# Optimization experiments

Measured on AMD Instinct MI355X. Metric: run time of the kernel, lower is better.

Reference implementation:

```python
import jax, jax.numpy as jnp
import numpy as np
from jax import lax


def conv2d(x, w, b, pad):
    # x: NCHW, w: OIHW
    out = lax.conv_general_dilated(x, w, (1, 1), [(pad, pad), (pad, pad)],
                                   dimension_numbers=('NCHW', 'OIHW', 'NCHW'))
    return out + b[None, :, None, None]


def traj_grid_sample(ps, gx, gy):
    """Faithful F.grid_sample (5D, trilinear, zeros padding, align_corners=False)
    applied to ps expanded along a depth axis of size L. Since every depth slice
    of the expanded input equals ps, we gather 2D from ps and fold the z-axis
    interpolation weights / bounds mask in analytically (no (B,C,L,H,W) expand).
    ps: (B,C,H,W); gx, gy: (B,L,H,W) pixel-coordinate flow fields."""
    B, C, H, W = ps.shape
    L = gx.shape[1]
    dt = ps.dtype
    # the original normalizes to [-1,1] assuming align_corners-style ranges
    gxn = gx / (W - 1) * 2 - 1
    gyn = gy / (H - 1) * 2 - 1
    gzn = jnp.arange(1, L + 1, dtype=dt) / (L - 1) * 2 - 1  # (L,)
    # torch grid_sample default align_corners=False unnormalization
    ix = ((gxn + 1) * W - 1) / 2
    iy = ((gyn + 1) * H - 1) / 2
    iz = jnp.broadcast_to((((gzn + 1) * L - 1) / 2)[None, :, None, None], ix.shape)
    x0 = jnp.floor(ix)
    y0 = jnp.floor(iy)
    z0 = jnp.floor(iz)
    bidx = jnp.arange(B)[:, None, None, None]
    out = jnp.zeros((B, L, H, W, C), dtype=dt)
    for dz in (0.0, 1.0):
        zc = z0 + dz
        wz = 1.0 - jnp.abs(iz - zc)
        mz = (zc >= 0) & (zc <= L - 1)
        for dy in (0.0, 1.0):
            yc = y0 + dy
            wy = 1.0 - jnp.abs(iy - yc)
            my = (yc >= 0) & (yc <= H - 1)
            yci = jnp.clip(yc, 0, H - 1).astype(jnp.int32)
            for dx in (0.0, 1.0):
                xc = x0 + dx
                wx = 1.0 - jnp.abs(ix - xc)
                mx = (xc >= 0) & (xc <= W - 1)
                xci = jnp.clip(xc, 0, W - 1).astype(jnp.int32)
                w = wz * wy * wx * (mz & my & mx).astype(dt)  # (B,L,H,W)
                val = ps[bidx, :, yci, xci]  # (B,L,H,W,C)
                out = out + val * w[..., None]
    return jnp.transpose(out, (0, 4, 1, 2, 3))  # (B,C,L,H,W)


def reference(x, prev_state, sub_w1, sub_b1, sub_w2, sub_b2,
              reset_w, reset_b, update_w, update_b, out_w, out_b,
              reset_ww, reset_wb, update_ww, update_wb, out_ww, out_wb):
    B, Ch, H, W = prev_state.shape
    L = sub_w2.shape[0] // 2
    # subCNN: flow generation
    s = jnp.concatenate([x, prev_state], axis=1)
    o = jax.nn.relu(conv2d(s, sub_w1, sub_b1, 2))
    o = jax.nn.relu(conv2d(o, sub_w2, sub_b2, 2))
    M = traj_grid_sample(prev_state, o[:, :L], o[:, L:])  # (B,Ch,L,H,W)
    Mf = M.reshape(B, Ch * L, H, W)  # view(B, C*L, H, W)
    update = jax.nn.sigmoid(conv2d(x, update_w, update_b, 1) + conv2d(Mf, update_ww, update_wb, 0))
    reset = jax.nn.sigmoid(conv2d(x, reset_w, reset_b, 1) + conv2d(Mf, reset_ww, reset_wb, 0))
    v = conv2d(x, out_w, out_b, 1) + reset * conv2d(Mf, out_ww, out_wb, 0)
    out_inputs = jnp.where(v >= 0, v, 0.2 * v)  # leaky_relu(0.2)
    return prev_state * update + out_inputs * (1.0 - update)


def setup_inputs() -> dict:
    key = jax.random.key(0)
    ks = jax.random.split(key, 12)
    B, Cin, Ch, L, H, W = 4, 8, 96, 13, 96, 96
    rn = lambda k, shape, s=0.05: jax.random.normal(k, shape, dtype=jnp.float32) * s
    z = lambda n: jnp.zeros((n,), jnp.float32)
    return {
        'x': rn(ks[0], (B, Cin, H, W), 1.0),
        'prev_state': rn(ks[1], (B, Ch, H, W), 1.0),
        'sub_w1': rn(ks[2], (32, Cin + Ch, 5, 5)), 'sub_b1': z(32),
        'sub_w2': rn(ks[3], (2 * L, 32, 5, 5)), 'sub_b2': z(2 * L),
        'reset_w': rn(ks[4], (Ch, Cin, 3, 3)), 'reset_b': z(Ch),
        'update_w': rn(ks[5], (Ch, Cin, 3, 3)), 'update_b': z(Ch),
        'out_w': rn(ks[6], (Ch, Cin, 3, 3)), 'out_b': z(Ch),
        'reset_ww': rn(ks[7], (Ch, Ch * L, 1, 1)), 'reset_wb': z(Ch),
        'update_ww': rn(ks[8], (Ch, Ch * L, 1, 1)), 'update_wb': z(Ch),
        'out_ww': rn(ks[9], (Ch, Ch * L, 1, 1)), 'out_wb': z(Ch),
    }
```

## Files before the change

### kernel.cpp

```cpp
#include <hip/hip_runtime.h>
#include <hip/hip_bf16.h>

#define HW 9216

typedef unsigned short ushort;
typedef unsigned int   uint;
typedef __attribute__((ext_vector_type(4))) float f32x4;
typedef __attribute__((ext_vector_type(4))) uint  u32x4;
typedef __attribute__((ext_vector_type(4))) int   i32x4;
typedef __attribute__((ext_vector_type(8))) short s16x8;

__device__ float  g_o1[4*32*HW];
__device__ float  g_q [2*4*26*HW];
__device__ __align__(16) float g_ht[4*HW*96];
__device__ __align__(16) ushort g_chi[4*(size_t)HW*128];
__device__ __align__(16) ushort g_clo[4*(size_t)HW*128];
__device__ __align__(16) ushort g_w1b[28*4*2048];
__device__ __align__(16) ushort g_b[18*39*512];
__device__ __align__(16) float  g_urv[2304*288*16];

__device__ __forceinline__ ushort f2b(float f){
  uint x = __float_as_uint(f);
  return (ushort)((x + 0x7FFFu + ((x >> 16) & 1u)) >> 16);
}
__device__ __forceinline__ float b2f(ushort h){
  return __uint_as_float(((uint)h) << 16);
}

__global__ void pack_b_k(const float* __restrict__ uww, const float* __restrict__ rww,
                         const float* __restrict__ vww){
  int i = blockIdx.x*256 + threadIdx.x;
  if (i >= 3*96*1248) return;
  int gate = i / (96*1248); int rem = i % (96*1248);
  int oc = rem / 1248;      int kp = rem % 1248;
  int l = kp / 96, c = kp % 96;
  const float* src = (gate == 0) ? uww : ((gate == 1) ? rww : vww);
  float v = src[oc*1248 + c*13 + l];
  int n  = gate*96 + oc;
  int nt = n >> 4, nl = n & 15;
  int kb = kp >> 5, kk = kp & 31;
  g_b[(nt*39 + kb)*512 + nl*32 + kk] = f2b(v);
}

__global__ void pack_w1b_k(const float* __restrict__ w1){
  int i = blockIdx.x*256 + threadIdx.x;
  if (i >= 25*4*1024) return;
  int tap = i >> 12;
  int cb  = (i >> 10) & 3;
  int oc  = (i >> 5) & 31;
  int kk  = i & 31;
  int ci  = cb*32 + kk;
  float w = (ci < 104) ? w1[oc*2600 + ci*25 + tap] : 0.f;
  ushort h = f2b(w);
  float rem = w - b2f(h);
  int base = ((tap*4 + cb) << 11) + (oc >> 4)*512 + (oc & 15)*32 + kk;
  g_w1b[base]        = h;
  g_w1b[base + 1024] = f2b(rem);
}

__global__ __launch_bounds__(256) void transpose_k(const float* __restrict__ hp,
                                                   const float* __restrict__ x){
  __shared__ float tile[32][33];
  int s0 = blockIdx.x*32;
  int b  = blockIdx.z;
  int t  = threadIdx.x;
  if (blockIdx.y < 3){
    int c0 = blockIdx.y*32;
    for (int i = t; i < 32*32; i += 256){
      int c = i >> 5, s = i & 31;
      tile[c][s] = hp[((size_t)(b*96 + c0 + c))*HW + s0 + s];
    }
    __syncthreads();
    for (int i = t; i < 32*32; i += 256){
      int s = i >> 5, c = i & 31;
      float v = tile[c][s];
      size_t px = (size_t)b*HW + s0 + s;
      g_ht[px*96 + c0 + c] = v;
      ushort h = f2b(v);
      g_chi[px*128 + 8 + c0 + c] = h;
      g_clo[px*128 + 8 + c0 + c] = f2b(v - b2f(h));
    }
  } else {
    for (int i = t; i < 8*32; i += 256){
      int c = i >> 5, s = i & 31;
      tile[c][s] = x[((size_t)(b*8 + c))*HW + s0 + s];
    }
    __syncthreads();
    for (int i = t; i < 32*8; i += 256){
      int s = i >> 3, c = i & 7;
      float v = tile[c][s];
      size_t px = (size_t)b*HW + s0 + s;
      ushort h = f2b(v);
      g_chi[px*128 + c] = h;
      g_clo[px*128 + c] = f2b(v - b2f(h));
    }
  }
}

__global__ __launch_bounds__(256) void conv1_mfma_k(const float* __restrict__ b1){
  __shared__ __align__(16) ushort sh[2*160*128];
  int t = threadIdx.x;
  int w = t >> 6, lane = t & 63;
  int nl = lane & 15, q = lane >> 4;
  int rt = blockIdx.x / 6, ct = blockIdx.x % 6;
  int b  = blockIdx.z;
  int r0 = rt*4, c0 = ct*16;
  const size_t pbase = (size_t)b*HW;

  #pragma unroll
  for (int i = 0; i < 20; i++){
    int idx = i*256 + t;
    int half = (i >= 10) ? 1 : 0;
    int rem = idx - half*2560;
    int px = rem >> 4, ci = rem & 15;
    int cs = ci ^ (px & 15);
    int r = px / 20, c = px - r*20;
    int gr = r0 + r - 2, gc = c0 + c - 2;
    f32x4 v = (f32x4){0.f,0.f,0.f,0.f};
    if ((unsigned)gr < 96u && (unsigned)gc < 96u){
      const ushort* src = half ? g_clo : g_chi;
      v = *(const f32x4*)(src + ((pbase + (size_t)(gr*96 + gc)) << 7) + cs*8);
    }
    *(f32x4*)((char*)sh + (size_t)idx*16) = v;
  }
  __syncthreads();

  int kxA[7], kyA[7], tpA[7];
  #pragma unroll
  for (int i = 0; i < 7; i++){
    int tp  = 7*w + i;
    int tpc = (tp > 24) ? 24 : tp;
    kyA[i] = tpc / 5;
    kxA[i] = tpc - kyA[i]*5;
    tpA[i] = tp;
  }
  int foff = nl*32 + q*8;

  f32x4 acc[4][2];
  #pragma unroll
  for (int mr = 0; mr < 4; mr++){
    acc[mr][0] = (f32x4){0.f,0.f,0.f,0.f};
    acc[mr][1] = (f32x4){0.f,0.f,0.f,0.f};
  }

  for (int cb = 0; cb < 4; cb++){
    const ushort* bpc = g_w1b + ((size_t)cb << 11);
    s16x8 bq[3][4];
#define LOADB(slot, i) { const ushort* bp = bpc + ((size_t)tpA[i] << 13); \
    bq[slot][0] = *(const s16x8*)(bp + foff); \
    bq[slot][1] = *(const s16x8*)(bp + 512 + foff); \
    bq[slot][2] = *(const s16x8*)(bp + 1024 + foff); \
    bq[slot][3] = *(const s16x8*)(bp + 1536 + foff); }
    LOADB(0, 0); LOADB(1, 1);

    #pragma unroll
    for (int i = 0; i < 7; i++){
      if (i < 5) LOADB((i + 2) % 3, i + 2);
      int ky = kyA[i], kx = kxA[i];
      int chq = cb*4 + q;
      s16x8 ah[4], al[4];
      #pragma unroll
      for (int mr = 0; mr < 4; mr++){
        int px  = (mr + ky)*20 + kx + nl;
        int off = px*256 + (((chq ^ (px & 15))) << 4);
        ah[mr] = *(const s16x8*)((const char*)sh + off);
        al[mr] = *(const s16x8*)((const char*)sh + 40960 + off);
      }
      const int cur = i % 3;
      #pragma unroll
      for (int mr = 0; mr < 4; mr++){
        acc[mr][0] = __builtin_amdgcn_mfma_f32_16x16x32_bf16(ah[mr], bq[cur][0], acc[mr][0], 0,0,0);
        acc[mr][1] = __builtin_amdgcn_mfma_f32_16x16x32_bf16(ah[mr], bq[cur][1], acc[mr][1], 0,0,0);
      }
      #pragma unroll
      for (int mr = 0; mr < 4; mr++){
        acc[mr][0] = __builtin_amdgcn_mfma_f32_16x16x32_bf16(al[mr], bq[cur][0], acc[mr][0], 0,0,0);
        acc[mr][1] = __builtin_amdgcn_mfma_f32_16x16x32_bf16(al[mr], bq[cur][1], acc[mr][1], 0,0,0);
      }
      #pragma unroll
      for (int mr = 0; mr < 4; mr++){
        acc[mr][0] = __builtin_amdgcn_mfma_f32_16x16x32_bf16(ah[mr], bq[cur][2], acc[mr][0], 0,0,0);
        acc[mr][1] = __builtin_amdgcn_mfma_f32_16x16x32_bf16(ah[mr], bq[cur][3], acc[mr][1], 0,0,0);
      }
    }
#undef LOADB
  }

  __syncthreads();
  float* red = (float*)sh;
  #pragma unroll
  for (int mr = 0; mr < 4; mr++)
    #pragma unroll
    for (int nt = 0; nt < 2; nt++)
      *(f32x4*)&red[(((mr*2 + nt)*4 + w) << 8) + lane*4] = acc[mr][nt];
  __syncthreads();

  int mr = w;
  #pragma unroll
  for (int nt = 0; nt < 2; nt++){
    f32x4 s = (f32x4){0.f,0.f,0.f,0.f};
    #pragma unroll
    for (int ww = 0; ww < 4; ww++)
      s += *(f32x4*)&red[(((mr*2 + nt)*4 + ww) << 8) + lane*4];
    int oc = nt*16 + nl;
    float bias = b1[oc];
    s.x = fmaxf(s.x + bias, 0.f); s.y = fmaxf(s.y + bias, 0.f);
    s.z = fmaxf(s.z + bias, 0.f); s.w = fmaxf(s.w + bias, 0.f);
    *(f32x4*)(g_o1 + ((size_t)(b*32 + oc))*HW + (size_t)(r0 + mr)*96 + c0 + q*4) = s;
  }
}

__global__ __launch_bounds__(256) void conv2_k(const float* __restrict__ wt2,
                                               const float* __restrict__ b2){
  __shared__ __align__(16) float in_sh[8][20][24];
  __shared__ __align__(16) float w_sh[8][25][32];
  int tile = blockIdx.x;
  int kg   = blockIdx.y;
  int b    = blockIdx.z;
  int row0 = (tile / 6) * 16, col0 = (tile % 6) * 16;
  int t = threadIdx.x;
  int og  = t >> 5;
  int pos = t & 31;
  int row = pos >> 1, x0 = (pos & 1)*8;

  float acc[8][4];
  #pragma unroll
  for (int j = 0; j < 8; j++)
    #pragma unroll
    for (int o = 0; o < 4; o++) acc[j][o] = 0.f;

  for (int cc = 0; cc < 2; cc++){
    __syncthreads();
    for (int idx = t; idx < 8*20*24; idx += 256){
      int i = idx / 480, rem = idx % 480;
      int r = rem / 24, c = rem % 24;
      int gr = row0 + r - 2, gc = col0 + c - 2;
      float v = 0.f;
      if ((unsigned)gr < 96u && (unsigned)gc < 96u){
        int ci = kg*16 + cc*8 + i;
        v = g_o1[(b*32 + ci)*HW + gr*96 + gc];
      }
      in_sh[i][r][c] = v;
    }
    for (int idx = t; idx < 8*25*32; idx += 256){
      int i = idx / 800, rem = idx % 800;
      int tap = rem / 32, oc = rem % 32;
      int ci = kg*16 + cc*8 + i;
      w_sh[i][tap][oc] = (oc < 26) ? wt2[oc*800 + ci*25 + tap] : 0.f;
    }
    __syncthreads();

    for (int i = 0; i < 8; i++){
      #pragma unroll
      for (int ky = 0; ky < 5; ky++){
        const float* rp = &in_sh[i][row + ky][x0];
        f32x4 s0 = *(const f32x4*)(rp);
        f32x4 s1 = *(const f32x4*)(rp + 4);
        f32x4 s2 = *(const f32x4*)(rp + 8);
        float seg[12] = {s0.x,s0.y,s0.z,s0.w, s1.x,s1.y,s1.z,s1.w, s2.x,s2.y,s2.z,s2.w};
        #pragma unroll
        for (int kx = 0; kx < 5; kx++){
          f32x4 wv = *(const f32x4*)&w_sh[i][ky*5 + kx][og*4];
          #pragma unroll
          for (int j = 0; j < 8; j++){
            float a = seg[kx + j];
            acc[j][0] += a*wv.x; acc[j][1] += a*wv.y;
            acc[j][2] += a*wv.z; acc[j][3] += a*wv.w;
          }
        }
      }
    }
  }

  int rg = row0 + row, cg = col0 + x0;
  #pragma unroll
  for (int o = 0; o < 4; o++){
    int slot = og*4 + o;
    if (slot < 26){
      float bias = (kg == 0) ? b2[slot] : 0.f;
      float* d = g_q + (size_t)kg*4*26*HW + ((size_t)(b*26 + slot))*HW + rg*96 + cg;
      #pragma unroll
      for (int j = 0; j < 8; j++) d[j] = acc[j][o] + bias;
    }
  }
}

__global__ __launch_bounds__(256) void gemm_k(){
  __shared__ __align__(16) ushort Bsh[18*512];
  __shared__ __align__(16) float cw4[13][64][4];
  __shared__ __align__(16) int   co4[13][64][4];
  int t = threadIdx.x;
  int w = t >> 6, lane = t & 63;
  int nl = lane & 15, quad = lane >> 4;
  int blk = blockIdx.x;
  int b   = blk / 144;
  int pbase0 = (blk % 144) * 64;
  int pt  = blk*4 + w;

  const int NQ = 4*26*HW;
  for (int idx = t; idx < 832; idx += 256){
    int l = idx >> 6, m = idx & 63;
    int p = pbase0 + m;
    float gx = fmaxf(g_q[(b*26 + l     )*HW + p] + g_q[NQ + (b*26 + l     )*HW + p], 0.f);
    float gy = fmaxf(g_q[(b*26 + 13 + l)*HW + p] + g_q[NQ + (b*26 + 13 + l)*HW + p], 0.f);
    float ix = gx * (96.f/95.f) - 0.5f;
    float iy = gy * (96.f/95.f) - 0.5f;
    float iz = (float)(l+1) * (13.f/12.f) - 0.5f;
    float z0 = floorf(iz);
    float zf = 0.f;
    #pragma unroll
    for (int dz = 0; dz < 2; dz++){
      float zc = z0 + (float)dz;
      float wz = 1.f - fabsf(iz - zc);
      if (zc >= 0.f && zc <= 12.f) zf += wz;
    }
    float x0f = floorf(ix), y0f = floorf(iy);
    #pragma unroll
    for (int dy = 0; dy < 2; dy++){
      float yc = y0f + (float)dy;
      float wy = 1.f - fabsf(iy - yc);
      bool  my = (yc >= 0.f) && (yc <= 95.f);
      int  yci = min(max((int)yc, 0), 95);
      #pragma unroll
      for (int dx = 0; dx < 2; dx++){
        float xc = x0f + (float)dx;
        float wx = 1.f - fabsf(ix - xc);
        bool  mx = (xc >= 0.f) && (xc <= 95.f);
        int  xci = min(max((int)xc, 0), 95);
        cw4[l][m][dy*2+dx] = (mx && my) ? zf*wy*wx : 0.f;
        co4[l][m][dy*2+dx] = yci*96 + xci;
      }
    }
  }

  f32x4 acc[18];
  #pragma unroll
  for (int nt = 0; nt < 18; nt++) acc[nt] = (f32x4){0.f,0.f,0.f,0.f};

  const uint* Bg = reinterpret_cast<const uint*>(g_b);
  uint* Bs32 = (uint*)Bsh;
  const float* hb = g_ht + (size_t)b*HW*96 + quad*8;
  int mloc = w*16 + nl;

  int l = 0, kb3 = 0;
  for (int kb = 0; kb < 39; kb++){
    __syncthreads();
    f32x4 wv = *(const f32x4*)cw4[l][mloc];
    i32x4 ov = *(const i32x4*)co4[l][mloc];
    const float* hc = hb + kb3*32;
    const float* p0 = hc + (size_t)ov.x*96;
    const float* p1 = hc + (size_t)ov.y*96;
    const float* p2 = hc + (size_t)ov.z*96;
    const float* p3 = hc + (size_t)ov.w*96;
    f32x4 v0a = *(const f32x4*)(p0), v0b = *(const f32x4*)(p0 + 4);
    f32x4 v1a = *(const f32x4*)(p1), v1b = *(const f32x4*)(p1 + 4);
    f32x4 v2a = *(const f32x4*)(p2), v2b = *(const f32x4*)(p2 + 4);
    f32x4 v3a = *(const f32x4*)(p3), v3b = *(const f32x4*)(p3 + 4);
    #pragma unroll
    for (int u = 0; u < 18; u++){
      int idx = u*256 + t;
      Bs32[idx] = Bg[(idx >> 8)*39*256 + kb*256 + (idx & 255)];
    }
    __syncthreads();
    f32x4 aA = wv.x*v0a + wv.y*v1a + wv.z*v2a + wv.w*v3a;
    f32x4 aB = wv.x*v0b + wv.y*v1b + wv.z*v2b + wv.w*v3b;
    union { u32x4 u; s16x8 s; } cv;
    cv.u.x = (uint)f2b(aA.x) | ((uint)f2b(aA.y) << 16);
    cv.u.y = (uint)f2b(aA.z) | ((uint)f2b(aA.w) << 16);
    cv.u.z = (uint)f2b(aB.x) | ((uint)f2b(aB.y) << 16);
    cv.u.w = (uint)f2b(aB.z) | ((uint)f2b(aB.w) << 16);
    s16x8 a = cv.s;
    #pragma unroll
    for (int nt = 0; nt < 18; nt++){
      s16x8 bf = *(const s16x8*)&Bsh[nt*512 + nl*32 + quad*8];
      acc[nt] = __builtin_amdgcn_mfma_f32_16x16x32_bf16(a, bf, acc[nt], 0, 0, 0);
    }
    kb3++; if (kb3 == 3){ kb3 = 0; l++; }
  }

  float* dst = g_urv + (size_t)pt*4608;
  #pragma unroll
  for (int nt = 0; nt < 18; nt++)
    *(f32x4*)&dst[(nt*16 + nl)*16 + quad*4] = acc[nt];
}

__global__ __launch_bounds__(256) void gate_k(const float* __restrict__ x,
                        const float* __restrict__ hp,
                        const float* __restrict__ uw, const float* __restrict__ ub,
                        const float* __restrict__ rw, const float* __restrict__ rb,
                        const float* __restrict__ vw, const float* __restrict__ vb,
                        const float* __restrict__ uwb, const float* __restrict__ rwb,
                        const float* __restrict__ vwb, float* __restrict__ out){
  int p  = blockIdx.x*256 + threadIdx.x;
  int oc = blockIdx.y;
  int b  = blockIdx.z;
  int h = p/96, w = p%96;
  float xU = ub[oc], xR = rb[oc], xV = vb[oc];
  const float* xb = x + b*8*HW;
  for (int ky = 0; ky < 3; ky++){
    int r = h+ky-1;
    if ((unsigned)r >= 96u) continue;
    for (int kx = 0; kx < 3; kx++){
      int c = w+kx-1;
      if ((unsigned)c >= 96u) continue;
      int off = r*96 + c;
      int wo  = ky*3 + kx;
      #pragma unroll
      for (int ic = 0; ic < 8; ic++){
        float a = xb[ic*HW + off];
        xU += a * uw[oc*72 + ic*9 + wo];
        xR += a * rw[oc*72 + ic*9 + wo];
        xV += a * vw[oc*72 + ic*9 + wo];
      }
    }
  }
  int pt = b*576 + (p >> 4), px = p & 15;
  const float* ur = g_urv + (size_t)pt*4608 + px;
  float gU = ur[(0*96 + oc)*16] + uwb[oc];
  float gR = ur[(1*96 + oc)*16] + rwb[oc];
  float gV = ur[(2*96 + oc)*16] + vwb[oc];
  float u = 1.f / (1.f + __expf(-(xU + gU)));
  float r = 1.f / (1.f + __expf(-(xR + gR)));
  float v = xV + r * gV;
  float oi = (v >= 0.f) ? v : 0.2f*v;
  float h0 = hp[(b*96 + oc)*HW + p];
  out[(b*96 + oc)*HW + p] = h0*u + oi*(1.f - u);
}

extern "C" void kernel_launch(void* const* d_in, const int* in_sizes, int n_in,
                              void* d_out, int out_size, void* d_ws, size_t ws_size,
                              hipStream_t stream){
  const float* x    = (const float*)d_in[0];
  const float* hp   = (const float*)d_in[1];
  const float* sw1  = (const float*)d_in[2];
  const float* sb1  = (const float*)d_in[3];
  const float* sw2  = (const float*)d_in[4];
  const float* sb2  = (const float*)d_in[5];
  const float* rw   = (const float*)d_in[6];
  const float* rb   = (const float*)d_in[7];
  const float* uw   = (const float*)d_in[8];
  const float* ub   = (const float*)d_in[9];
  const float* vw   = (const float*)d_in[10];
  const float* vb   = (const float*)d_in[11];
  const float* rww  = (const float*)d_in[12];
  const float* rwb  = (const float*)d_in[13];
  const float* uww  = (const float*)d_in[14];
  const float* uwb  = (const float*)d_in[15];
  const float* vww  = (const float*)d_in[16];
  const float* vwb  = (const float*)d_in[17];

  pack_b_k    <<<dim3((3*96*1248 + 255)/256), dim3(256), 0, stream>>>(uww, rww, vww);
  pack_w1b_k  <<<dim3((25*4*1024 + 255)/256), dim3(256), 0, stream>>>(sw1);
  transpose_k <<<dim3(288, 4, 4), dim3(256), 0, stream>>>(hp, x);
  conv1_mfma_k<<<dim3(144, 1, 4), dim3(256), 0, stream>>>(sb1);
  conv2_k     <<<dim3(36, 2, 4), dim3(256), 0, stream>>>(sw2, sb2);
  gemm_k      <<<dim3(576),      dim3(256), 0, stream>>>();
  gate_k      <<<dim3(36, 96, 4), dim3(256), 0, stream>>>(x, hp,
               uw, ub, rw, rb, vw, vb, uwb, rwb, vwb, (float*)d_out);
}
```

Before: 389.1 us.

## Software-pipeline B tile and gather loads into registers in trajectory GEMM loop

Rewrites the trajectory-sample GEMM K loop to prefetch the next K block's packed weights and gathered hidden-state values into registers while the current block's MFMAs run, double-buffered via a macro-unrolled loop. It also repacks the weight layout so each lane reads a contiguous 16-byte B fragment from shared memory, and stores to LDS with 8-byte writes. The intent is to hide global load latency behind compute and reduce LDS bank conflicts, at the cost of more registers and possible occupancy loss.

```diff
diff --git a/kernel.cpp b/kernel.cpp
--- a/kernel.cpp
+++ b/kernel.cpp
@@ -6,6 +6,7 @@
 typedef unsigned short ushort;
 typedef unsigned int   uint;
 typedef __attribute__((ext_vector_type(4))) float f32x4;
+typedef __attribute__((ext_vector_type(2))) uint  u32x2;
 typedef __attribute__((ext_vector_type(4))) uint  u32x4;
 typedef __attribute__((ext_vector_type(4))) int   i32x4;
 typedef __attribute__((ext_vector_type(8))) short s16x8;
@@ -39,7 +40,7 @@
   int n  = gate*96 + oc;
   int nt = n >> 4, nl = n & 15;
   int kb = kp >> 5, kk = kp & 31;
-  g_b[(nt*39 + kb)*512 + nl*32 + kk] = f2b(v);
+  g_b[(nt*39 + kb)*512 + ((kk >> 3)*16 + nl)*8 + (kk & 7)] = f2b(v);
 }
 
 __global__ void pack_w1b_k(const float* __restrict__ w1){
@@ -337,46 +338,85 @@
   #pragma unroll
   for (int nt = 0; nt < 18; nt++) acc[nt] = (f32x4){0.f,0.f,0.f,0.f};
 
-  const uint* Bg = reinterpret_cast<const uint*>(g_b);
-  uint* Bs32 = (uint*)Bsh;
+  const u32x2* Bg8 = reinterpret_cast<const u32x2*>(g_b);
   const float* hb = g_ht + (size_t)b*HW*96 + quad*8;
   int mloc = w*16 + nl;
 
-  int l = 0, kb3 = 0;
-  for (int kb = 0; kb < 39; kb++){
-    __syncthreads();
-    f32x4 wv = *(const f32x4*)cw4[l][mloc];
-    i32x4 ov = *(const i32x4*)co4[l][mloc];
-    const float* hc = hb + kb3*32;
-    const float* p0 = hc + (size_t)ov.x*96;
-    const float* p1 = hc + (size_t)ov.y*96;
-    const float* p2 = hc + (size_t)ov.z*96;
-    const float* p3 = hc + (size_t)ov.w*96;
-    f32x4 v0a = *(const f32x4*)(p0), v0b = *(const f32x4*)(p0 + 4);
-    f32x4 v1a = *(const f32x4*)(p1), v1b = *(const f32x4*)(p1 + 4);
-    f32x4 v2a = *(const f32x4*)(p2), v2b = *(const f32x4*)(p2 + 4);
-    f32x4 v3a = *(const f32x4*)(p3), v3b = *(const f32x4*)(p3 + 4);
-    #pragma unroll
-    for (int u = 0; u < 18; u++){
-      int idx = u*256 + t;
-      Bs32[idx] = Bg[(idx >> 8)*39*256 + kb*256 + (idx & 255)];
-    }
-    __syncthreads();
-    f32x4 aA = wv.x*v0a + wv.y*v1a + wv.z*v2a + wv.w*v3a;
-    f32x4 aB = wv.x*v0b + wv.y*v1b + wv.z*v2b + wv.w*v3b;
-    union { u32x4 u; s16x8 s; } cv;
-    cv.u.x = (uint)f2b(aA.x) | ((uint)f2b(aA.y) << 16);
-    cv.u.y = (uint)f2b(aA.z) | ((uint)f2b(aA.w) << 16);
-    cv.u.z = (uint)f2b(aB.x) | ((uint)f2b(aB.y) << 16);
-    cv.u.w = (uint)f2b(aB.z) | ((uint)f2b(aB.w) << 16);
-    s16x8 a = cv.s;
-    #pragma unroll
-    for (int nt = 0; nt < 18; nt++){
-      s16x8 bf = *(const s16x8*)&Bsh[nt*512 + nl*32 + quad*8];
-      acc[nt] = __builtin_amdgcn_mfma_f32_16x16x32_bf16(a, bf, acc[nt], 0, 0, 0);
-    }
-    kb3++; if (kb3 == 3){ kb3 = 0; l++; }
-  }
+  f32x4 gA[8], gB[8], wA, wB;
+  u32x2 sA[9], sB[9];
+
+  #pragma unroll
+  for (int u = 0; u < 9; u++){
+    int idx8 = u*256 + t;
+    sA[u] = Bg8[((idx8 >> 7)*39 + 0)*128 + (idx8 & 127)];
+  }
+  __syncthreads();
+
+  {
+    wA = *(const f32x4*)cw4[0][mloc];
+    i32x4 ov_ = *(const i32x4*)co4[0][mloc];
+    const float* q0_ = hb + (size_t)ov_.x*96;
+    const float* q1_ = hb + (size_t)ov_.y*96;
+    const float* q2_ = hb + (size_t)ov_.z*96;
+    const float* q3_ = hb + (size_t)ov_.w*96;
+    gA[0]=*(const f32x4*)q0_; gA[1]=*(const f32x4*)(q0_+4);
+    gA[2]=*(const f32x4*)q1_; gA[3]=*(const f32x4*)(q1_+4);
+    gA[4]=*(const f32x4*)q2_; gA[5]=*(const f32x4*)(q2_+4);
+    gA[6]=*(const f32x4*)q3_; gA[7]=*(const f32x4*)(q3_+4);
+  }
+  int ln = 0, k3n = 1;
+
+#define BODY(KB, GC, WC, GN, WN, SC, SN, PF) { \
+  if (PF){ \
+    _Pragma("unroll") \
+    for (int u = 0; u < 9; u++){ \
+      int idx8 = u*256 + t; \
+      SN[u] = Bg8[((idx8 >> 7)*39 + (KB) + 1)*128 + (idx8 & 127)]; \
+    } \
+    WN = *(const f32x4*)cw4[ln][mloc]; \
+    i32x4 ov_ = *(const i32x4*)co4[ln][mloc]; \
+    const float* hc_ = hb + k3n*32; \
+    const float* q0_ = hc_ + (size_t)ov_.x*96; \
+    const float* q1_ = hc_ + (size_t)ov_.y*96; \
+    const float* q2_ = hc_ + (size_t)ov_.z*96; \
+    const float* q3_ = hc_ + (size_t)ov_.w*96; \
+    GN[0]=*(const f32x4*)q0_; GN[1]=*(const f32x4*)(q0_+4); \
+    GN[2]=*(const f32x4*)q1_; GN[3]=*(const f32x4*)(q1_+4); \
+    GN[4]=*(const f32x4*)q2_; GN[5]=*(const f32x4*)(q2_+4); \
+    GN[6]=*(const f32x4*)q3_; GN[7]=*(const f32x4*)(q3_+4); \
+    k3n++; if (k3n == 3){ k3n = 0; ln++; } \
+  } \
+  _Pragma("unroll") \
+  for (int u = 0; u < 9; u++){ \
+    int idx8 = u*256 + t; \
+    *(u32x2*)((char*)Bsh + idx8*8) = SC[u]; \
+  } \
+  f32x4 aA = WC.x*GC[0] + WC.y*GC[2] + WC.z*GC[4] + WC.w*GC[6]; \
+  f32x4 aB = WC.x*GC[1] + WC.y*GC[3] + WC.z*GC[5] + WC.w*GC[7]; \
+  union { u32x4 u4; s16x8 s8v; } cv_; \
+  cv_.u4.x = (uint)f2b(aA.x) | ((uint)f2b(aA.y) << 16); \
+  cv_.u4.y = (uint)f2b(aA.z) | ((uint)f2b(aA.w) << 16); \
+  cv_.u4.z = (uint)f2b(aB.x) | ((uint)f2b(aB.y) << 16); \
+  cv_.u4.w = (uint)f2b(aB.z) | ((uint)f2b(aB.w) << 16); \
+  asm volatile("s_waitcnt lgkmcnt(0)" ::: "memory"); \
+  __builtin_amdgcn_s_barrier(); \
+  asm volatile("" ::: "memory"); \
+  _Pragma("unroll") \
+  for (int nt = 0; nt < 18; nt++){ \
+    s16x8 bf = *(const s16x8*)((const char*)Bsh + nt*1024 + lane*16); \
+    acc[nt] = __builtin_amdgcn_mfma_f32_16x16x32_bf16(cv_.s8v, bf, acc[nt], 0, 0, 0); \
+  } \
+  asm volatile("" ::: "memory"); \
+  __builtin_amdgcn_s_barrier(); \
+  asm volatile("" ::: "memory"); \
+}
+
+  for (int kb = 0; kb < 38; kb += 2){
+    BODY(kb,     gA, wA, gB, wB, sA, sB, 1);
+    BODY(kb + 1, gB, wB, gA, wA, sB, sA, 1);
+  }
+  BODY(38, gA, wA, gB, wB, sA, sB, 0);
+#undef BODY
 
   float* dst = g_urv + (size_t)pt*4608;
   #pragma unroll
```

Result: faster. 380.8 us (-2.1%).
